# Kernel optimization log

Hardware: AMD Instinct MI355X
Metric: run time of the kernel (lower is better)

Reference implementation:

```python
import jax, jax.numpy as jnp
import numpy as np

VOCAB = 90
EMBED = 8
HIDDEN = 256
B, S = 256, 512


def setup_inputs() -> dict:
    key = jax.random.key(0)
    ks = jax.random.split(key, 12)
    s_e = 1.0 / np.sqrt(HIDDEN)
    inp = {
        "x": jax.random.randint(ks[0], (B, S), 0, VOCAB),
        "emb": jax.random.normal(ks[1], (VOCAB, EMBED), jnp.float32),
        # layer 0 (input size EMBED)
        "Wih0": jax.random.uniform(ks[2], (4 * HIDDEN, EMBED), jnp.float32, -s_e, s_e),
        "Whh0": jax.random.uniform(ks[3], (4 * HIDDEN, HIDDEN), jnp.float32, -s_e, s_e),
        "bih0": jax.random.uniform(ks[4], (4 * HIDDEN,), jnp.float32, -s_e, s_e),
        "bhh0": jax.random.uniform(ks[5], (4 * HIDDEN,), jnp.float32, -s_e, s_e),
        # layer 1 (input size HIDDEN)
        "Wih1": jax.random.uniform(ks[6], (4 * HIDDEN, HIDDEN), jnp.float32, -s_e, s_e),
        "Whh1": jax.random.uniform(ks[7], (4 * HIDDEN, HIDDEN), jnp.float32, -s_e, s_e),
        "bih1": jax.random.uniform(ks[8], (4 * HIDDEN,), jnp.float32, -s_e, s_e),
        "bhh1": jax.random.uniform(ks[9], (4 * HIDDEN,), jnp.float32, -s_e, s_e),
        # final projection
        "Wfc": jax.random.uniform(ks[10], (VOCAB, HIDDEN), jnp.float32, -s_e, s_e),
        "bfc": jax.random.uniform(ks[11], (VOCAB,), jnp.float32, -s_e, s_e),
    }
    return inp


def _lstm_layer(x, Wih, Whh, bih, bhh):
    # x: [B, S, Din] -> [B, S, H]. PyTorch gate order: i, f, g, o.
    H = Whh.shape[1]
    # precompute input contributions for all timesteps: [S, B, 4H]
    xg = jnp.einsum('bsd,gd->sbg', x, Wih) + (bih + bhh)

    def step(carry, xg_t):
        h, c = carry
        gates = xg_t + h @ Whh.T  # [B, 4H]
        i, f, g, o = jnp.split(gates, 4, axis=-1)
        i = jax.nn.sigmoid(i)
        f = jax.nn.sigmoid(f)
        g = jnp.tanh(g)
        o = jax.nn.sigmoid(o)
        c = f * c + i * g
        h = o * jnp.tanh(c)
        return (h, c), h

    Bc = x.shape[0]
    h0 = jnp.zeros((Bc, H), x.dtype)
    c0 = jnp.zeros((Bc, H), x.dtype)
    _, hs = jax.lax.scan(step, (h0, c0), xg)  # hs: [S, B, H]
    return jnp.transpose(hs, (1, 0, 2))


def reference(x, emb, Wih0, Whh0, bih0, bhh0, Wih1, Whh1, bih1, bhh1, Wfc, bfc):
    embedded = emb[x]                                   # [B, S, E]
    h1 = _lstm_layer(embedded, Wih0, Whh0, bih0, bhh0)  # [B, S, H]
    h2 = _lstm_layer(h1, Wih1, Whh1, bih1, bhh1)        # [B, S, H]
    logits = jnp.einsum('bsh,vh->bsv', h2, Wfc) + bfc   # [B, S, V]
    return logits
```

## Files before the change

### kernel.cpp

```cpp
#include <hip/hip_runtime.h>
#include <math.h>

typedef _Float16 f16;
typedef _Float16 f16x8 __attribute__((ext_vector_type(8)));
typedef _Float16 f16x4 __attribute__((ext_vector_type(4)));
typedef float f32x4 __attribute__((ext_vector_type(4)));

#define NS     512
#define NG     1024
#define NV     90
#define TC     64

#define R_LDS_BYTES 155648

__device__ __forceinline__ float sgf(float x) {
    return __builtin_amdgcn_rcpf(1.f + __builtin_amdgcn_exp2f(-1.44269504089f * x));
}
__device__ __forceinline__ float thf(float x) {
    return 2.f * __builtin_amdgcn_rcpf(1.f + __builtin_amdgcn_exp2f(-2.88539008178f * x)) - 1.f;
}



__global__ void build_t0p(const float* __restrict__ emb, const float* __restrict__ wih0,
                          const float* __restrict__ bih0, const float* __restrict__ bhh0,
                          f16* __restrict__ t0p) {
    int v = blockIdx.x, hid = threadIdx.x;
    __shared__ float e[8];
    if (hid < 8) e[hid] = emb[v * 8 + hid];
    __syncthreads();
    f16x4 o;
    #pragma unroll
    for (int g = 0; g < 4; ++g) {
        int n = g * 256 + hid;
        float s = bih0[n] + bhh0[n];
        #pragma unroll
        for (int k = 0; k < 8; ++k) s += e[k] * wih0[n * 8 + k];
        o[g] = (f16)s;
    }
    *(f16x4*)&t0p[((size_t)v * 256 + hid) * 4] = o;
}

__global__ void pack_rw(const float* __restrict__ W, f16* __restrict__ Wp) {
    int gid = blockIdx.x * 256 + threadIdx.x;
    int l = gid & 63, f = (gid >> 6) & 127, w = gid >> 13;
    int kt = f & 7, g = (f >> 3) & 3, jt = f >> 5;
    int n = g * 256 + w * 64 + jt * 16 + (l & 15);
    int k = kt * 32 + (l >> 4) * 8;
    f16x8 v;
    #pragma unroll
    for (int e = 0; e < 8; ++e) v[e] = (f16)W[n * 256 + k + e];
    *(f16x8*)&Wp[(size_t)gid * 8] = v;
}

__global__ void pack_fc(const float* __restrict__ Wfc, f16* __restrict__ Wp) {
    int gid = blockIdx.x * 256 + threadIdx.x;
    int l = gid & 63, kt = (gid >> 6) & 7, nt = gid >> 9;
    int n = nt * 16 + (l & 15);
    int k = kt * 32 + (l >> 4) * 8;
    f16x8 v;
    #pragma unroll
    for (int e = 0; e < 8; ++e) v[e] = (n < NV) ? (f16)Wfc[n * 256 + k + e] : (f16)0.f;
    *(f16x8*)&Wp[(size_t)gid * 8] = v;
}

template<int LAYER>
__device__ __forceinline__ void rnn_body(const f16* __restrict__ Wp, const int* __restrict__ x,
                                         const f16* __restrict__ T0p, const f16* __restrict__ xgc,
                                         f16* __restrict__ hdump, float* __restrict__ cst,
                                         f16* __restrict__ hst, int t0, int bp, char* smem) {
    f16* hb = (f16*)smem;
    const int tid = threadIdx.x;
    const int w = tid >> 6, l = tid & 63, l15 = l & 15, lq = l >> 4;
    const int R0 = bp * 2;

    const f16* wgl = Wp + ((size_t)w * 128) * 512 + l * 8;
    f16* wlds = (f16*)(smem + 16384 + w * 34816);

    #pragma unroll
    for (int fi = 0; fi < 34; ++fi) {
        int f = (fi < 32) ? ((fi >> 1) * 8 + 6 + (fi & 1)) : ((14 + (fi - 32)) * 8 + 5);
        *(f16x8*)&wlds[fi * 512 + l * 8] = *(const f16x8*)&wgl[(size_t)f * 512];
    }

    f32x4 w_a[64];
    #pragma unroll
    for (int q = 0; q < 16; ++q)
        #pragma unroll
        for (int kt = 0; kt < 4; ++kt)
            w_a[q * 4 + kt] = *(const f32x4*)&wgl[(size_t)(q * 8 + kt) * 512];
    #pragma unroll
    for (int i = 0; i < 64; ++i) asm volatile("" : "+a"(w_a[i]));

    f32x4 w_v[30];
    #pragma unroll
    for (int q = 0; q < 16; ++q) w_v[q] = *(const f32x4*)&wgl[(size_t)(q * 8 + 4) * 512];
    #pragma unroll
    for (int q = 0; q < 14; ++q) w_v[16 + q] = *(const f32x4*)&wgl[(size_t)(q * 8 + 5) * 512];
    #pragma unroll
    for (int i = 0; i < 30; ++i) asm volatile("" : "+v"(w_v[i]));

    #pragma unroll
    for (int i = 0; i < 4; ++i) *(uint4*)(smem + tid * 64 + i * 16) = (uint4){0, 0, 0, 0};
    __syncthreads();

    float c[8];
    #pragma unroll
    for (int i = 0; i < 8; ++i) c[i] = 0.f;
    if (t0 > 0) {
        #pragma unroll
        for (int i = 0; i < 2; ++i) {
            int idx = tid + i * 256;
            int r = idx >> 8, hid = idx & 255;
            hb[r * 256 + (hid ^ (32 * r))] = hst[(size_t)bp * 512 + r * 256 + hid];
        }
        if (lq == 0) {
            const float* cp = cst + (((size_t)bp * 4 + w) * 16 + l15) * 8;
            #pragma unroll
            for (int i = 0; i < 8; ++i) c[i] = cp[i];
        }
    }
    __syncthreads();

    f16x4 ivc0 = {}, ivc1 = {};
    int xv0 = 0, xv1 = 0, xvn0 = 0, xvn1 = 0;
    if (lq == 0) {
        const int hid0 = w * 64 + l15;
        if constexpr (LAYER == 0) {
            xv0 = x[(R0 + 0) * NS + t0];
            xv1 = x[(R0 + 1) * NS + t0];
            ivc0 = *(const f16x4*)&T0p[((size_t)xv0 * 256 + hid0) * 4];
            ivc1 = *(const f16x4*)&T0p[((size_t)xv1 * 256 + hid0) * 4];
        } else {
            ivc0 = *(const f16x4*)&xgc[((size_t)(R0 + 0) * 256 + hid0) * 4];
            ivc1 = *(const f16x4*)&xgc[((size_t)(R0 + 1) * 256 + hid0) * 4];
        }
    }

    for (int s = 0; s < TC; ++s) {
        const int t = t0 + s;
        const int rb = (s & 1) * 4096, wb = rb ^ 4096;

        f16x8 a[8];
        #pragma unroll
        for (int kt = 0; kt < 8; ++kt)
            a[kt] = *(const f16x8*)&hb[rb + l15 * 256 + ((kt * 32 + lq * 8) ^ (32 * (l15 & 7)))];

        if constexpr (LAYER == 0) {
            if (lq == 0) {
                int tn = (t + 1 < NS) ? t + 1 : NS - 1;
                xvn0 = x[(R0 + 0) * NS + tn];
                xvn1 = x[(R0 + 1) * NS + tn];
            }
        }

        #pragma unroll
        for (int jt = 0; jt < 4; ++jt) {
            f16x4 ivn0 = {}, ivn1 = {};
            if (lq == 0) {
                if (jt < 3) {
                    const int hidN = w * 64 + (jt + 1) * 16 + l15;
                    if constexpr (LAYER == 0) {
                        ivn0 = *(const f16x4*)&T0p[((size_t)xv0 * 256 + hidN) * 4];
                        ivn1 = *(const f16x4*)&T0p[((size_t)xv1 * 256 + hidN) * 4];
                    } else {
                        ivn0 = *(const f16x4*)&xgc[(((size_t)s * 256 + R0 + 0) * 256 + hidN) * 4];
                        ivn1 = *(const f16x4*)&xgc[(((size_t)s * 256 + R0 + 1) * 256 + hidN) * 4];
                    }
                } else {
                    const int sn = (s + 1 < TC) ? s + 1 : s;
                    const int hid0 = w * 64 + l15;
                    if constexpr (LAYER == 0) {
                        ivn0 = *(const f16x4*)&T0p[((size_t)xvn0 * 256 + hid0) * 4];
                        ivn1 = *(const f16x4*)&T0p[((size_t)xvn1 * 256 + hid0) * 4];
                    } else {
                        ivn0 = *(const f16x4*)&xgc[(((size_t)sn * 256 + R0 + 0) * 256 + hid0) * 4];
                        ivn1 = *(const f16x4*)&xgc[(((size_t)sn * 256 + R0 + 1) * 256 + hid0) * 4];
                    }
                }
            }

            f32x4 acc[4];
            #pragma unroll
            for (int g = 0; g < 4; ++g) acc[g] = (f32x4){0.f, 0.f, 0.f, 0.f};

            #pragma unroll
            for (int kt = 0; kt < 8; ++kt) {
                #pragma unroll
                for (int g = 0; g < 4; ++g) {
                    const int q = jt * 4 + g;
                    f16x8 bfr;
                    if (kt < 4)                 bfr = __builtin_bit_cast(f16x8, w_a[q * 4 + kt]);
                    else if (kt == 4)           bfr = __builtin_bit_cast(f16x8, w_v[q]);
                    else if (kt == 5 && q < 14) bfr = __builtin_bit_cast(f16x8, w_v[16 + q]);
                    else if (kt == 5)           bfr = *(const f16x8*)&wlds[(32 + (q - 14)) * 512 + l * 8];
                    else                        bfr = *(const f16x8*)&wlds[(q * 2 + (kt - 6)) * 512 + l * 8];
                    acc[g] = __builtin_amdgcn_mfma_f32_16x16x32_f16(a[kt], bfr, acc[g], 0, 0, 0);
                }
            }

            if (lq == 0) {
                #pragma unroll
                for (int r = 0; r < 2; ++r) {
                    const f16x4 iv = r ? ivc1 : ivc0;
                    float gi = acc[0][r] + (float)iv[0];
                    float gf = acc[1][r] + (float)iv[1];
                    float gg = acc[2][r] + (float)iv[2];
                    float go = acc[3][r] + (float)iv[3];
                    float si = sgf(gi), sf = sgf(gf), tg = thf(gg), so = sgf(go);
                    const int ci = jt * 2 + r;
                    c[ci] = sf * c[ci] + si * tg;
                    float h = so * thf(c[ci]);
                    const int hid = w * 64 + jt * 16 + l15;
                    hb[wb + r * 256 + (hid ^ (32 * r))] = (f16)h;
                    hdump[((size_t)s * 256 + R0 + r) * 256 + hid] = (f16)h;
                }
            }
            ivc0 = ivn0; ivc1 = ivn1;
            if constexpr (LAYER == 0) {
                if (jt == 3) { xv0 = xvn0; xv1 = xvn1; }
            }
        }
        __syncthreads();
    }
    if (lq == 0) {
        float* cp = cst + (((size_t)bp * 4 + w) * 16 + l15) * 8;
        #pragma unroll
        for (int i = 0; i < 8; ++i) cp[i] = c[i];
    }
    #pragma unroll
    for (int i = 0; i < 2; ++i) {
        int idx = tid + i * 256;
        int r = idx >> 8, hid = idx & 255;
        hst[(size_t)bp * 512 + r * 256 + hid] = hb[r * 256 + (hid ^ (32 * r))];
    }
}

__global__ __launch_bounds__(256, 1)
void fused_rnn(const f16* __restrict__ Wp0, const f16* __restrict__ Wp1,
               const int* __restrict__ x, const f16* __restrict__ T0p,
               const f16* __restrict__ xgc, f16* __restrict__ h1g, f16* __restrict__ h2g,
               float* __restrict__ cst0, float* __restrict__ cst1,
               f16* __restrict__ hst0, f16* __restrict__ hst1,
               int t0l0, int do0, int do1) {
    extern __shared__ char smem[];
    if (blockIdx.x < 128) {
        if (do0) rnn_body<0>(Wp0, x, T0p, nullptr, h1g, cst0, hst0, t0l0, blockIdx.x, smem);
    } else {
        if (do1) rnn_body<1>(Wp1, nullptr, nullptr, xgc, h2g, cst1, hst1, t0l0 - TC, blockIdx.x - 128, smem);
    }
}

__launch_bounds__(256, 1)
__global__ void xg1_gemm(const f16* __restrict__ h1g, const f16* __restrict__ Wxp,
                         const float* __restrict__ bih1, const float* __restrict__ bhh1,
                         f16* __restrict__ xgc) {
    const int tid = threadIdx.x, wv = tid >> 6, l = tid & 63, l15 = l & 15, lq = l >> 4;
    const int bid = blockIdx.x, bg = bid & 15, ns = (bid >> 4) & 3, tcc = bid >> 6;

    f16x8 bf[4][8];
    #pragma unroll
    for (int g = 0; g < 4; ++g)
        #pragma unroll
        for (int kt = 0; kt < 8; ++kt)
            bf[g][kt] = *(const f16x8*)&Wxp[((size_t)(ns * 128 + (wv * 4 + g) * 8 + kt) * 64 + l) * 8];
    float bs[4];
    #pragma unroll
    for (int g = 0; g < 4; ++g) {
        int n = g * 256 + ns * 64 + wv * 16 + l15;
        bs[g] = bih1[n] + bhh1[n];
    }
    const int hid = ns * 64 + wv * 16 + l15;

    for (int tt = 0; tt < 16; ++tt) {
        int s = tcc * 16 + tt;
        f16x8 a[8];
        #pragma unroll
        for (int kt = 0; kt < 8; ++kt)
            a[kt] = *(const f16x8*)&h1g[((size_t)s * 256 + bg * 16 + l15) * 256 + kt * 32 + lq * 8];
        f32x4 acc[4];
        #pragma unroll
        for (int g = 0; g < 4; ++g) acc[g] = (f32x4){bs[g], bs[g], bs[g], bs[g]};
        #pragma unroll
        for (int kt = 0; kt < 8; ++kt)
            #pragma unroll
            for (int g = 0; g < 4; ++g)
                acc[g] = __builtin_amdgcn_mfma_f32_16x16x32_f16(a[kt], bf[g][kt], acc[g], 0, 0, 0);
        #pragma unroll
        for (int r = 0; r < 4; ++r) {
            f16x4 o = { (f16)acc[0][r], (f16)acc[1][r], (f16)acc[2][r], (f16)acc[3][r] };
            int row = bg * 16 + lq * 4 + r;
            *(f16x4*)&xgc[(((size_t)s * 256 + row) * 256 + hid) * 4] = o;
        }
    }
}

__launch_bounds__(256, 1)
__global__ void fc_out(const f16* __restrict__ h2g, const f16* __restrict__ Wfcp,
                       const float* __restrict__ bfc, float* __restrict__ out, int t0) {
    const int tid = threadIdx.x, wv = tid >> 6, l = tid & 63, l15 = l & 15, lq = l >> 4;
    const int bid = blockIdx.x, bg = bid & 15, tb = bid >> 4;
    const int s = tb * 4 + wv;

    f16x8 bf[6][8];
    #pragma unroll
    for (int nt = 0; nt < 6; ++nt)
        #pragma unroll
        for (int kt = 0; kt < 8; ++kt)
            bf[nt][kt] = *(const f16x8*)&Wfcp[((size_t)(nt * 8 + kt) * 64 + l) * 8];
    float bb[6];
    #pragma unroll
    for (int nt = 0; nt < 6; ++nt) {
        int n = nt * 16 + l15;
        bb[nt] = (n < NV) ? bfc[n] : 0.f;
    }

    f16x8 a[8];
    #pragma unroll
    for (int kt = 0; kt < 8; ++kt)
        a[kt] = *(const f16x8*)&h2g[((size_t)s * 256 + bg * 16 + l15) * 256 + kt * 32 + lq * 8];
    f32x4 acc[6];
    #pragma unroll
    for (int nt = 0; nt < 6; ++nt) acc[nt] = (f32x4){bb[nt], bb[nt], bb[nt], bb[nt]};
    #pragma unroll
    for (int kt = 0; kt < 8; ++kt)
        #pragma unroll
        for (int nt = 0; nt < 6; ++nt)
            acc[nt] = __builtin_amdgcn_mfma_f32_16x16x32_f16(a[kt], bf[nt][kt], acc[nt], 0, 0, 0);
    #pragma unroll
    for (int nt = 0; nt < 6; ++nt) {
        int n = nt * 16 + l15;
        if (n < NV) {
            #pragma unroll
            for (int r = 0; r < 4; ++r)
                out[((size_t)(bg * 16 + lq * 4 + r) * NS + (t0 + s)) * NV + n] = acc[nt][r];
        }
    }
}

extern "C" void kernel_launch(void* const* d_in, const int* in_sizes, int n_in,
                              void* d_out, int out_size, void* d_ws, size_t ws_size,
                              hipStream_t stream) {
    const int*   x    = (const int*)  d_in[0];
    const float* emb  = (const float*)d_in[1];
    const float* wih0 = (const float*)d_in[2];
    const float* whh0 = (const float*)d_in[3];
    const float* bih0 = (const float*)d_in[4];
    const float* bhh0 = (const float*)d_in[5];
    const float* wih1 = (const float*)d_in[6];
    const float* whh1 = (const float*)d_in[7];
    const float* bih1 = (const float*)d_in[8];
    const float* bhh1 = (const float*)d_in[9];
    const float* wfc  = (const float*)d_in[10];
    const float* bfc  = (const float*)d_in[11];
    float* out = (float*)d_out;

    char* ws = (char*)d_ws;
    f16*   Wp0  = (f16*)(ws + 0);
    f16*   Wp1  = (f16*)(ws + 524288);
    f16*   Wxp  = (f16*)(ws + 1048576);
    f16*   Wfcp = (f16*)(ws + 1572864);
    f16*   T0p  = (f16*)(ws + 1622016);
    float* cst0 = (float*)(ws + 1806336);
    float* cst1 = (float*)(ws + 2068480);
    f16*   hst0 = (f16*)(ws + 2330624);
    f16*   hst1 = (f16*)(ws + 2461696);
    const size_t base = 2592768;

    f16* h1g = (f16*)(ws + base);
    f16* xgc = (f16*)(ws + base + (size_t)TC * 131072);
    f16* h2g = (f16*)(ws + base + (size_t)TC * 131072 + (size_t)TC * 524288);

    hipFuncSetAttribute(reinterpret_cast<const void*>(fused_rnn),
                        hipFuncAttributeMaxDynamicSharedMemorySize, R_LDS_BYTES);

    build_t0p<<<90, 256, 0, stream>>>(emb, wih0, bih0, bhh0, T0p);
    pack_rw<<<128, 256, 0, stream>>>(whh0, Wp0);
    pack_rw<<<128, 256, 0, stream>>>(whh1, Wp1);
    pack_rw<<<128, 256, 0, stream>>>(wih1, Wxp);
    pack_fc<<<12, 256, 0, stream>>>(wfc, Wfcp);

    const int NCH = NS / TC;
    for (int k = 0; k <= NCH; ++k) {
        fused_rnn<<<256, 256, R_LDS_BYTES, stream>>>(Wp0, Wp1, x, T0p, xgc, h1g, h2g,
                                                     cst0, cst1, hst0, hst1,
                                                     k * TC, (int)(k < NCH), (int)(k > 0));
        if (k < NCH) xg1_gemm<<<16 * 4 * (TC / 16), 256, 0, stream>>>(h1g, Wxp, bih1, bhh1, xgc);
        if (k > 0)   fc_out<<<16 * (TC / 4), 256, 0, stream>>>(h2g, Wfcp, bfc, out, (k - 1) * TC);
    }
}
```

Baseline: 1.978 ms.

## Batch hidden-state dumps per step, lighten step barrier, merge aux kernels

Instead of each lq==0 lane writing h to global memory inside the gate loop, all 256 threads copy the previous step's h from LDS to global at the start of the next step, with the final step written in the epilogue. The per-step __syncthreads is replaced by an explicit lgkmcnt wait plus s_barrier, so the barrier no longer waits on outstanding global stores. The xg1 GEMM and FC output kernels are merged into one launch, cutting launches per chunk. This adds LDS reads each step, and skipping the vmcnt wait relies on the later kernel boundary to order the global writes.

New measurement: 1.885 ms. 1.05x faster.

```diff
diff --git a/kernel.cpp b/kernel.cpp
--- a/kernel.cpp
+++ b/kernel.cpp
@@ -12,6 +12,13 @@
 #define TC     64
 
 #define R_LDS_BYTES 155648
+
+#define STEP_BARRIER() do {                                   \
+    asm volatile("s_waitcnt lgkmcnt(0)" ::: "memory");        \
+    __builtin_amdgcn_sched_barrier(0);                        \
+    __builtin_amdgcn_s_barrier();                             \
+    __builtin_amdgcn_sched_barrier(0);                        \
+} while (0)
 
 __device__ __forceinline__ float sgf(float x) {
     return __builtin_amdgcn_rcpf(1.f + __builtin_amdgcn_exp2f(-1.44269504089f * x));
@@ -145,6 +152,16 @@
         #pragma unroll
         for (int kt = 0; kt < 8; ++kt)
             a[kt] = *(const f16x8*)&hb[rb + l15 * 256 + ((kt * 32 + lq * 8) ^ (32 * (l15 & 7)))];
+
+        if (s > 0) {
+            #pragma unroll
+            for (int i = 0; i < 2; ++i) {
+                int idx = tid + i * 256;
+                int r = idx >> 8, hid = idx & 255;
+                hdump[((size_t)(s - 1) * 256 + R0 + r) * 256 + hid] =
+                    hb[rb + r * 256 + (hid ^ (32 * r))];
+            }
+        }
 
         if constexpr (LAYER == 0) {
             if (lq == 0) {
@@ -213,7 +230,6 @@
                     float h = so * thf(c[ci]);
                     const int hid = w * 64 + jt * 16 + l15;
                     hb[wb + r * 256 + (hid ^ (32 * r))] = (f16)h;
-                    hdump[((size_t)s * 256 + R0 + r) * 256 + hid] = (f16)h;
                 }
             }
             ivc0 = ivn0; ivc1 = ivn1;
@@ -221,7 +237,7 @@
                 if (jt == 3) { xv0 = xvn0; xv1 = xvn1; }
             }
         }
-        __syncthreads();
+        STEP_BARRIER();
     }
     if (lq == 0) {
         float* cp = cst + (((size_t)bp * 4 + w) * 16 + l15) * 8;
@@ -232,7 +248,9 @@
     for (int i = 0; i < 2; ++i) {
         int idx = tid + i * 256;
         int r = idx >> 8, hid = idx & 255;
-        hst[(size_t)bp * 512 + r * 256 + hid] = hb[r * 256 + (hid ^ (32 * r))];
+        f16 hv = hb[r * 256 + (hid ^ (32 * r))];
+        hdump[((size_t)(TC - 1) * 256 + R0 + r) * 256 + hid] = hv;
+        hst[(size_t)bp * 512 + r * 256 + hid] = hv;
     }
 }
 
@@ -251,12 +269,11 @@
     }
 }
 
-__launch_bounds__(256, 1)
-__global__ void xg1_gemm(const f16* __restrict__ h1g, const f16* __restrict__ Wxp,
-                         const float* __restrict__ bih1, const float* __restrict__ bhh1,
-                         f16* __restrict__ xgc) {
+__device__ __forceinline__ void xg1_body(const f16* __restrict__ h1g, const f16* __restrict__ Wxp,
+                                         const float* __restrict__ bih1, const float* __restrict__ bhh1,
+                                         f16* __restrict__ xgc, int bid) {
     const int tid = threadIdx.x, wv = tid >> 6, l = tid & 63, l15 = l & 15, lq = l >> 4;
-    const int bid = blockIdx.x, bg = bid & 15, ns = (bid >> 4) & 3, tcc = bid >> 6;
+    const int bg = bid & 15, ns = (bid >> 4) & 3, tcc = bid >> 6;
 
     f16x8 bf[4][8];
     #pragma unroll
@@ -295,11 +312,11 @@
     }
 }
 
-__launch_bounds__(256, 1)
-__global__ void fc_out(const f16* __restrict__ h2g, const f16* __restrict__ Wfcp,
-                       const float* __restrict__ bfc, float* __restrict__ out, int t0) {
+__device__ __forceinline__ void fc_body(const f16* __restrict__ h2g, const f16* __restrict__ Wfcp,
+                                        const float* __restrict__ bfc, float* __restrict__ out,
+                                        int t0, int bid) {
     const int tid = threadIdx.x, wv = tid >> 6, l = tid & 63, l15 = l & 15, lq = l >> 4;
-    const int bid = blockIdx.x, bg = bid & 15, tb = bid >> 4;
+    const int bg = bid & 15, tb = bid >> 4;
     const int s = tb * 4 + wv;
 
     f16x8 bf[6][8];
@@ -335,6 +352,19 @@
             for (int r = 0; r < 4; ++r)
                 out[((size_t)(bg * 16 + lq * 4 + r) * NS + (t0 + s)) * NV + n] = acc[nt][r];
         }
+    }
+}
+
+__global__ __launch_bounds__(256, 1)
+void aux_kernel(const f16* __restrict__ h1g, const f16* __restrict__ Wxp,
+                const float* __restrict__ bih1, const float* __restrict__ bhh1,
+                f16* __restrict__ xgc, const f16* __restrict__ h2g,
+                const f16* __restrict__ Wfcp, const float* __restrict__ bfc,
+                float* __restrict__ out, int t0fc, int doXg, int doFc) {
+    if (blockIdx.x < 256) {
+        if (doXg) xg1_body(h1g, Wxp, bih1, bhh1, xgc, blockIdx.x);
+    } else {
+        if (doFc) fc_body(h2g, Wfcp, bfc, out, t0fc, blockIdx.x - 256);
     }
 }
 
@@ -385,7 +415,7 @@
         fused_rnn<<<256, 256, R_LDS_BYTES, stream>>>(Wp0, Wp1, x, T0p, xgc, h1g, h2g,
                                                      cst0, cst1, hst0, hst1,
                                                      k * TC, (int)(k < NCH), (int)(k > 0));
-        if (k < NCH) xg1_gemm<<<16 * 4 * (TC / 16), 256, 0, stream>>>(h1g, Wxp, bih1, bhh1, xgc);
-        if (k > 0)   fc_out<<<16 * (TC / 4), 256, 0, stream>>>(h2g, Wfcp, bfc, out, (k - 1) * TC);
-    }
-}
+        aux_kernel<<<512, 256, 0, stream>>>(h1g, Wxp, bih1, bhh1, xgc, h2g, Wfcp, bfc,
+                                            out, (k - 1) * TC, (int)(k < NCH), (int)(k > 0));
+    }
+}
```
